# Kernel tuning notes

Measured on AMD Instinct MI355X. Metric: run time of the kernel, lower is better.

## Reference

```python
import jax, jax.numpy as jnp
import numpy as np

NX = 48
N_TILES = 6
C_IN = 16
H = 32            # node_hidden_channels
EH = 64           # edge_hidden_channels
N_STEPS = 4       # num_step_message_passing
N_NODES = N_TILES * NX * NX


def _build_edges(nx, n_tiles):
    # 4-neighbor (up/down/left/right, wraparound) connectivity per tile
    ii = np.arange(nx * nx, dtype=np.int32).reshape(nx, nx)
    srcs, dsts = [], []
    for t in range(n_tiles):
        off = t * nx * nx
        for ax, sh in ((0, 1), (0, -1), (1, 1), (1, -1)):
            srcs.append(off + np.roll(ii, sh, axis=ax).ravel())
            dsts.append(off + ii.ravel())
    return np.concatenate(srcs), np.concatenate(dsts)


def setup_inputs() -> dict:
    key = jax.random.key(0)
    ks = jax.random.split(key, 16)
    src_np, dst_np = _build_edges(NX, N_TILES)
    E = src_np.shape[0]  # 55296
    s = 0.1
    return {
        "in_node_feats": jax.random.normal(ks[0], (2, N_TILES, NX, NX, C_IN), jnp.float32),
        "edge_feats": jax.random.normal(ks[1], (E, 2), jnp.float32),
        "src": jnp.asarray(src_np, jnp.int32),
        "dst": jnp.asarray(dst_np, jnp.int32),
        # project_node_feats: Linear(C_IN,H) -> relu -> Linear(H,H)
        "pW1": jax.random.normal(ks[2], (C_IN, H), jnp.float32) * s,
        "pb1": jnp.zeros((H,), jnp.float32),
        "pW2": jax.random.normal(ks[3], (H, H), jnp.float32) * s,
        "pb2": jnp.zeros((H,), jnp.float32),
        # edge network: Linear(2,EH) -> relu -> Linear(EH, H*H)
        "eW1": jax.random.normal(ks[4], (2, EH), jnp.float32) * s,
        "eb1": jnp.zeros((EH,), jnp.float32),
        "eW2": jax.random.normal(ks[5], (EH, H * H), jnp.float32) * (s / 4.0),
        "eb2": jnp.zeros((H * H,), jnp.float32),
        # NNConv bias
        "conv_b": jnp.zeros((H,), jnp.float32),
        # GRU (single layer): gate order r, z, n (PyTorch)
        "gWih": jax.random.normal(ks[6], (3 * H, H), jnp.float32) * s,
        "gWhh": jax.random.normal(ks[7], (3 * H, H), jnp.float32) * s,
        "gbih": jnp.zeros((3 * H,), jnp.float32),
        "gbhh": jnp.zeros((3 * H,), jnp.float32),
    }


def reference(in_node_feats, edge_feats, src, dst,
              pW1, pb1, pW2, pb2, eW1, eb1, eW2, eb2,
              conv_b, gWih, gWhh, gbih, gbhh):
    shp = in_node_feats.shape           # (B, T, nx, ny, Cin)
    B = shp[0]
    N = shp[1] * shp[2] * shp[3]
    x = in_node_feats.reshape(B, N, shp[-1])
    # project node features
    x = jnp.maximum(x @ pW1 + pb1, 0.0) @ pW2 + pb2      # (B, N, H)
    # per-edge weight matrices (shared across batch and steps)
    We = jnp.maximum(edge_feats @ eW1 + eb1, 0.0) @ eW2 + eb2
    We = We.reshape(-1, H, H)                             # (E, H, H)
    h = x
    seg = jax.vmap(lambda m: jax.ops.segment_sum(m, dst, num_segments=N))
    for _ in range(N_STEPS):
        # NNConv: gather src feats, per-edge matmul, scatter-sum to dst, + bias
        msg = jnp.einsum('beh,eho->beo', x[:, src], We)   # (B, E, H)
        x = jnp.maximum(seg(msg) + conv_b, 0.0)           # relu(conv)
        # GRU cell (seq_len = 1)
        gx = x @ gWih.T + gbih
        gh = h @ gWhh.T + gbhh
        xr, xz, xn = jnp.split(gx, 3, axis=-1)
        hr, hz, hn = jnp.split(gh, 3, axis=-1)
        r = jax.nn.sigmoid(xr + hr)
        z = jax.nn.sigmoid(xz + hz)
        n = jnp.tanh(xn + r * hn)
        h = (1.0 - z) * n + z * h
        x = h
    return x.reshape(shp[:4] + (H,))
```

## Files before the change

### kernel.cpp

```cpp
#include <hip/hip_runtime.h>
#include <stdint.h>

constexpr int NB   = 2;
constexpr int NN   = 13824;
constexpr int NE   = 55296;
constexpr int H    = 32;
constexpr int EHID = 64;
constexpr int HH   = 1024;
constexpr int TILE = 2304;
constexpr int NXC  = 48;

typedef float f32x4 __attribute__((ext_vector_type(4)));
typedef short s16x8 __attribute__((ext_vector_type(8)));
typedef unsigned int u32x2 __attribute__((ext_vector_type(2)));
typedef __attribute__((address_space(1))) unsigned int as1_uint;
typedef __attribute__((address_space(3))) unsigned int as3_uint;

static __device__ __forceinline__ unsigned short f2bf(float f) {
    unsigned u = __float_as_uint(f);
    return (unsigned short)((u + 0x7fffu + ((u >> 16) & 1u)) >> 16);
}
static __device__ __forceinline__ void gload16(const void* g, void* l) {
    __builtin_amdgcn_global_load_lds((const as1_uint*)g, (as3_uint*)l, 16, 0, 0);
}
static __device__ __forceinline__ float sigf(float v) {
    return 1.0f / (1.0f + __expf(-v));
}
static __device__ __forceinline__ float tanhfast(float v) {
    return 1.0f - 2.0f / (1.0f + __expf(2.0f * v));
}

__global__ void __launch_bounds__(256)
k_prep(const float* __restrict__ ef, const float* __restrict__ eW1,
       const float* __restrict__ eb1, unsigned short* __restrict__ aB,
       const float* __restrict__ eW2, const float* __restrict__ eb2,
       unsigned short* __restrict__ BpT, float* __restrict__ eb2p) {
    int blk = blockIdx.x;
    if (blk < 13824) {
        int t = blk * 256 + threadIdx.x;
        int e = t >> 6, k = t & 63;
        float v = ef[e * 2] * eW1[k] + ef[e * 2 + 1] * eW1[64 + k] + eb1[k];
        aB[t] = f2bf(fmaxf(v, 0.f));
    } else {
        int idx = (blk - 13824) * 256 + threadIdx.x;
        int jp = idx & (HH - 1);
        int k  = idx >> 10;
        int src_col = (jp & 31) * 32 + (jp >> 5);
        BpT[jp * EHID + k] = f2bf(eW2[k * HH + src_col]);
        if (k == 0) eb2p[jp] = eb2[src_col];
    }
}

__global__ void __launch_bounds__(256)
k_gemm(const unsigned short* __restrict__ A, const unsigned short* __restrict__ Bt,
       const float* __restrict__ eb2p, unsigned short* __restrict__ C) {
    __shared__ unsigned char lds[32768] __attribute__((aligned(16)));
    const int tid  = threadIdx.x;
    const int wv   = tid >> 6;
    const int lane = tid & 63;
    const int lr   = lane & 15;
    const int lg   = lane >> 4;
    const int nb   = blockIdx.x;
    const int mb   = blockIdx.y;

    const unsigned char* Ag = (const unsigned char*)A  + (size_t)mb * 16384;
    const unsigned char* Bg = (const unsigned char*)Bt + (size_t)nb * 16384;

#pragma unroll
    for (int c = 0; c < 4; c++) {
        int fbase = (wv * 4 + c) * 1024;
        int f  = fbase + lane * 16;
        int sw = f ^ (((f >> 7) & 7) << 4);
        gload16(Ag + sw, lds + fbase);
        gload16(Bg + sw, lds + 16384 + fbase);
    }
    asm volatile("s_waitcnt vmcnt(0)" ::: "memory");
    __syncthreads();

    const int wm = wv >> 1, wn = wv & 1;
    f32x4 acc[4][4] = {};
#pragma unroll
    for (int kk = 0; kk < 2; kk++) {
        s16x8 af[4], bf[4];
#pragma unroll
        for (int i = 0; i < 4; i++) {
            int la = ((wm * 64 + i * 16 + lr) * 64 + kk * 32 + lg * 8) * 2;
            la ^= ((la >> 7) & 7) << 4;
            af[i] = *(const s16x8*)(lds + la);
            int lb = ((wn * 64 + i * 16 + lr) * 64 + kk * 32 + lg * 8) * 2;
            lb ^= ((lb >> 7) & 7) << 4;
            bf[i] = *(const s16x8*)(lds + 16384 + lb);
        }
#pragma unroll
        for (int i = 0; i < 4; i++)
#pragma unroll
            for (int j = 0; j < 4; j++)
                acc[i][j] = __builtin_amdgcn_mfma_f32_16x16x32_bf16(af[i], bf[j], acc[i][j], 0, 0, 0);
    }

#pragma unroll
    for (int j = 0; j < 4; j++) {
        int col = nb * 128 + wn * 64 + j * 16 + lr;
        float bias = eb2p[col];
#pragma unroll
        for (int i = 0; i < 4; i++) {
            int row0 = mb * 128 + wm * 64 + i * 16 + lg * 4;
#pragma unroll
            for (int r = 0; r < 4; r++)
                C[(size_t)(row0 + r) * HH + col] = f2bf(acc[i][j][r] + bias);
        }
    }
}

__global__ void __launch_bounds__(256)
k_proj(const float* __restrict__ in, const float* __restrict__ pW1,
       const float* __restrict__ pb1, const float* __restrict__ pW2,
       const float* __restrict__ pb2, float* __restrict__ S0,
       unsigned short* __restrict__ xb0,
       const float* __restrict__ gWih, const float* __restrict__ gWhh,
       unsigned short* __restrict__ gWb) {
    int blk = blockIdx.x;
    if (blk >= 3456) {
        int idx = (blk - 3456) * 256 + threadIdx.x;
        gWb[idx] = f2bf(idx < 3072 ? gWih[idx] : gWhh[idx - 3072]);
        return;
    }
    int t = blk * 256 + threadIdx.x;
    int p = t >> 5;
    int l = t & 31;
    float iv = (l < 16) ? in[p * 16 + l] : 0.f;
    float hid = pb1[l];
#pragma unroll
    for (int c = 0; c < 16; c++) hid = fmaf(__shfl(iv, c, 32), pW1[c * H + l], hid);
    hid = fmaxf(hid, 0.f);
    float out = pb2[l];
#pragma unroll
    for (int h = 0; h < 32; h++) out = fmaf(__shfl(hid, h, 32), pW2[h * H + l], out);
    S0[p * H + l]  = out;
    xb0[p * H + l] = f2bf(out);
}

__global__ void __launch_bounds__(256)
k_conv(const unsigned short* __restrict__ xb,
       const unsigned short* __restrict__ WeT,
       const float* __restrict__ conv_b,
       unsigned short* __restrict__ cval) {
    const int tid  = threadIdx.x;
    const int wv   = tid >> 6;
    const int l    = tid & 63;
    const int cl   = l & 15;
    const int kg   = l >> 4;
    const int bsel = cl & 1;
    const int n0   = (blockIdx.x * 4 + wv) * 8;

    f32x4 cb0 = *(const f32x4*)(conv_b + kg * 4);
    f32x4 cb1 = *(const f32x4*)(conv_b + 16 + kg * 4);

    for (int u = 0; u < 8; ++u) {
        int n = n0 + u;
        int t = n / TILE;
        int i = n - t * TILE;
        int r = i / NXC;
        int c = i - r * NXC;
        int bt = t * TILE;
        int rm = (r == 0) ? NXC - 1 : r - 1;
        int rp = (r == NXC - 1) ? 0 : r + 1;
        int cm = (c == 0) ? NXC - 1 : c - 1;
        int cp = (c == NXC - 1) ? 0 : c + 1;
        int s0 = bt + rm * NXC + c;
        int s1 = bt + rp * NXC + c;
        int s2 = bt + r * NXC + cm;
        int s3 = bt + r * NXC + cp;
        int ss[4] = {s0, s1, s2, s3};

        f32x4 a0 = {}, a1 = {};
#pragma unroll
        for (int k = 0; k < 4; ++k) {
            size_t e = (size_t)((t * 4 + k) * TILE + i);
            const unsigned short* wp = WeT + e * HH;
            s16x8 af0 = *(const s16x8*)(wp + cl * 32 + kg * 8);
            s16x8 af1 = *(const s16x8*)(wp + 512 + cl * 32 + kg * 8);
            s16x8 bfr = *(const s16x8*)(xb + ((size_t)(bsel * NN + ss[k])) * 32 + kg * 8);
            a0 = __builtin_amdgcn_mfma_f32_16x16x32_bf16(af0, bfr, a0, 0, 0, 0);
            a1 = __builtin_amdgcn_mfma_f32_16x16x32_bf16(af1, bfr, a1, 0, 0, 0);
        }
        if (cl < 2) {
            unsigned short* op = cval + ((size_t)(bsel * NN + n)) * 32 + kg * 4;
            u32x2 p0, p1;
            p0[0] = (unsigned)f2bf(fmaxf(a0[0] + cb0[0], 0.f)) |
                    ((unsigned)f2bf(fmaxf(a0[1] + cb0[1], 0.f)) << 16);
            p0[1] = (unsigned)f2bf(fmaxf(a0[2] + cb0[2], 0.f)) |
                    ((unsigned)f2bf(fmaxf(a0[3] + cb0[3], 0.f)) << 16);
            p1[0] = (unsigned)f2bf(fmaxf(a1[0] + cb1[0], 0.f)) |
                    ((unsigned)f2bf(fmaxf(a1[1] + cb1[1], 0.f)) << 16);
            p1[1] = (unsigned)f2bf(fmaxf(a1[2] + cb1[2], 0.f)) |
                    ((unsigned)f2bf(fmaxf(a1[3] + cb1[3], 0.f)) << 16);
            *(u32x2*)op        = p0;
            *(u32x2*)(op + 16) = p1;
        }
    }
}

__global__ void __launch_bounds__(256)
k_gru(const unsigned short* __restrict__ cval,
      const unsigned short* __restrict__ xbin,
      const float* __restrict__ hin,
      const unsigned short* __restrict__ gWb,
      const float* __restrict__ gbih, const float* __restrict__ gbhh,
      float* __restrict__ hout, unsigned short* __restrict__ xbout) {
    const int tid = threadIdx.x;
    const int wv  = tid >> 6;
    const int l   = tid & 63;
    const int cl  = l & 15;
    const int kg  = l >> 4;
    const int mt  = blockIdx.x * 4 + wv;

    s16x8 ax = *(const s16x8*)(cval + (size_t)mt * 512 + cl * 32 + kg * 8);
    s16x8 ah = *(const s16x8*)(xbin + (size_t)mt * 512 + cl * 32 + kg * 8);

    f32x4 accx[6], acch[6];
#pragma unroll
    for (int jb = 0; jb < 6; ++jb) {
        s16x8 wx = *(const s16x8*)(gWb + (jb * 16 + cl) * 32 + kg * 8);
        s16x8 wh = *(const s16x8*)(gWb + 3072 + (jb * 16 + cl) * 32 + kg * 8);
        f32x4 z0 = {};
        f32x4 z1 = {};
        accx[jb] = __builtin_amdgcn_mfma_f32_16x16x32_bf16(ax, wx, z0, 0, 0, 0);
        acch[jb] = __builtin_amdgcn_mfma_f32_16x16x32_bf16(ah, wh, z1, 0, 0, 0);
    }

    float bihR[2] = {gbih[cl],      gbih[16 + cl]};
    float bihZ[2] = {gbih[32 + cl], gbih[48 + cl]};
    float bihN[2] = {gbih[64 + cl], gbih[80 + cl]};
    float bhhR[2] = {gbhh[cl],      gbhh[16 + cl]};
    float bhhZ[2] = {gbhh[32 + cl], gbhh[48 + cl]};
    float bhhN[2] = {gbhh[64 + cl], gbhh[80 + cl]};

#pragma unroll
    for (int hb = 0; hb < 2; ++hb) {
        const float* hp = hin  + (size_t)mt * 512 + kg * 128 + hb * 16 + cl;
        float*       op = hout + (size_t)mt * 512 + kg * 128 + hb * 16 + cl;
        unsigned short* xp = xbout + (size_t)mt * 512 + kg * 128 + hb * 16 + cl;
#pragma unroll
        for (int ri = 0; ri < 4; ++ri) {
            float rg = sigf(accx[hb][ri] + acch[hb][ri] + bihR[hb] + bhhR[hb]);
            float zg = sigf(accx[2 + hb][ri] + acch[2 + hb][ri] + bihZ[hb] + bhhZ[hb]);
            float ng = tanhfast((accx[4 + hb][ri] + bihN[hb]) +
                                rg * (acch[4 + hb][ri] + bhhN[hb]));
            float ho = hp[ri * 32];
            float hn = fmaf(zg, ho - ng, ng);
            op[ri * 32] = hn;
            xp[ri * 32] = f2bf(hn);
        }
    }
}

extern "C" void kernel_launch(void* const* d_in, const int* in_sizes, int n_in,
                              void* d_out, int out_size, void* d_ws, size_t ws_size,
                              hipStream_t stream) {
    const float* in_nodes = (const float*)d_in[0];
    const float* ef       = (const float*)d_in[1];
    const float* pW1      = (const float*)d_in[4];
    const float* pb1      = (const float*)d_in[5];
    const float* pW2      = (const float*)d_in[6];
    const float* pb2      = (const float*)d_in[7];
    const float* eW1      = (const float*)d_in[8];
    const float* eb1      = (const float*)d_in[9];
    const float* eW2      = (const float*)d_in[10];
    const float* eb2      = (const float*)d_in[11];
    const float* convb    = (const float*)d_in[12];
    const float* gWih     = (const float*)d_in[13];
    const float* gWhh     = (const float*)d_in[14];
    const float* gbih     = (const float*)d_in[15];
    const float* gbhh     = (const float*)d_in[16];

    unsigned char* ws = (unsigned char*)d_ws;
    unsigned short* WeT  = (unsigned short*)(ws + 0ull);
    unsigned short* aB   = (unsigned short*)(ws + 113246208ull);
    unsigned short* xb0  = (unsigned short*)(ws + 113246208ull);
    unsigned short* xb1  = (unsigned short*)(ws + 115015680ull);
    unsigned short* cval = (unsigned short*)(ws + 116785152ull);
    unsigned short* gWb  = (unsigned short*)(ws + 118554624ull);
    unsigned short* BpT  = (unsigned short*)(ws + 120324096ull);
    float*          eb2p = (float*)         (ws + 120455168ull);
    float*          S0   = (float*)         (ws + 120459264ull);
    float*          S1   = (float*)         (ws + 123998208ull);

    k_prep<<<13824 + 256, 256, 0, stream>>>(ef, eW1, eb1, aB, eW2, eb2, BpT, eb2p);
    dim3 g3(8, 432);
    k_gemm<<<g3, 256, 0, stream>>>(aB, BpT, eb2p, WeT);
    k_proj<<<3456 + 24, 256, 0, stream>>>(in_nodes, pW1, pb1, pW2, pb2, S0, xb0,
                                          gWih, gWhh, gWb);

    float* out = (float*)d_out;
    k_conv<<<432, 256, 0, stream>>>(xb0, WeT, convb, cval);
    k_gru <<<432, 256, 0, stream>>>(cval, xb0, S0, gWb, gbih, gbhh, S1, xb1);
    k_conv<<<432, 256, 0, stream>>>(xb1, WeT, convb, cval);
    k_gru <<<432, 256, 0, stream>>>(cval, xb1, S1, gWb, gbih, gbhh, S0, xb0);
    k_conv<<<432, 256, 0, stream>>>(xb0, WeT, convb, cval);
    k_gru <<<432, 256, 0, stream>>>(cval, xb0, S0, gWb, gbih, gbhh, S1, xb1);
    k_conv<<<432, 256, 0, stream>>>(xb1, WeT, convb, cval);
    k_gru <<<432, 256, 0, stream>>>(cval, xb1, S1, gWb, gbih, gbhh, out, xb0);
}
```

Baseline: 246.6 us.

## Fuse NNConv and GRU per step, vectorize prep, stage GEMM output through LDS

```diff
diff --git a/kernel.cpp b/kernel.cpp
--- a/kernel.cpp
+++ b/kernel.cpp
@@ -13,12 +13,16 @@
 typedef float f32x4 __attribute__((ext_vector_type(4)));
 typedef short s16x8 __attribute__((ext_vector_type(8)));
 typedef unsigned int u32x2 __attribute__((ext_vector_type(2)));
+typedef unsigned int u32x4 __attribute__((ext_vector_type(4)));
 typedef __attribute__((address_space(1))) unsigned int as1_uint;
 typedef __attribute__((address_space(3))) unsigned int as3_uint;
 
 static __device__ __forceinline__ unsigned short f2bf(float f) {
     unsigned u = __float_as_uint(f);
     return (unsigned short)((u + 0x7fffu + ((u >> 16) & 1u)) >> 16);
+}
+static __device__ __forceinline__ unsigned packbf(float lo, float hi) {
+    return (unsigned)f2bf(lo) | ((unsigned)f2bf(hi) << 16);
 }
 static __device__ __forceinline__ void gload16(const void* g, void* l) {
     __builtin_amdgcn_global_load_lds((const as1_uint*)g, (as3_uint*)l, 16, 0, 0);
@@ -36,23 +40,36 @@
        const float* __restrict__ eW2, const float* __restrict__ eb2,
        unsigned short* __restrict__ BpT, float* __restrict__ eb2p) {
     int blk = blockIdx.x;
-    if (blk < 13824) {
+    if (blk < 3456) {
         int t = blk * 256 + threadIdx.x;
-        int e = t >> 6, k = t & 63;
-        float v = ef[e * 2] * eW1[k] + ef[e * 2 + 1] * eW1[64 + k] + eb1[k];
-        aB[t] = f2bf(fmaxf(v, 0.f));
+        int e = t >> 4, kq = (t & 15) * 4;
+        float f0 = ef[e * 2], f1 = ef[e * 2 + 1];
+        u32x2 w;
+#pragma unroll
+        for (int q = 0; q < 2; q++) {
+            int k = kq + q * 2;
+            float v0 = fmaxf(f0 * eW1[k]     + f1 * eW1[64 + k]     + eb1[k],     0.f);
+            float v1 = fmaxf(f0 * eW1[k + 1] + f1 * eW1[64 + k + 1] + eb1[k + 1], 0.f);
+            w[q] = packbf(v0, v1);
+        }
+        *(u32x2*)(aB + e * 64 + kq) = w;
     } else {
-        int idx = (blk - 13824) * 256 + threadIdx.x;
-        int jp = idx & (HH - 1);
-        int k  = idx >> 10;
+        int t = (blk - 3456) * 256 + threadIdx.x;
+        int jp = t >> 4, kq = (t & 15) * 4;
         int src_col = (jp & 31) * 32 + (jp >> 5);
-        BpT[jp * EHID + k] = f2bf(eW2[k * HH + src_col]);
-        if (k == 0) eb2p[jp] = eb2[src_col];
+        u32x2 w;
+#pragma unroll
+        for (int q = 0; q < 2; q++) {
+            int k = kq + q * 2;
+            w[q] = packbf(eW2[k * HH + src_col], eW2[(k + 1) * HH + src_col]);
+        }
+        *(u32x2*)(BpT + jp * 64 + kq) = w;
+        if (kq == 0) eb2p[jp] = eb2[src_col];
     }
 }
 
 __global__ void __launch_bounds__(256)
-k_gemm(const unsigned short* __restrict__ A, const unsigned short* __restrict__ Bt,
+k_gemm(const unsigned short* __restrict__ Bp, const unsigned short* __restrict__ Ae,
        const float* __restrict__ eb2p, unsigned short* __restrict__ C) {
     __shared__ unsigned char lds[32768] __attribute__((aligned(16)));
     const int tid  = threadIdx.x;
@@ -60,11 +77,11 @@
     const int lane = tid & 63;
     const int lr   = lane & 15;
     const int lg   = lane >> 4;
-    const int nb   = blockIdx.x;
-    const int mb   = blockIdx.y;
-
-    const unsigned char* Ag = (const unsigned char*)A  + (size_t)mb * 16384;
-    const unsigned char* Bg = (const unsigned char*)Bt + (size_t)nb * 16384;
+    const int jbt  = blockIdx.x;
+    const int ebt  = blockIdx.y;
+
+    const unsigned char* Ag = (const unsigned char*)Bp + (size_t)jbt * 16384;
+    const unsigned char* Bg = (const unsigned char*)Ae + (size_t)ebt * 16384;
 
 #pragma unroll
     for (int c = 0; c < 4; c++) {
@@ -98,17 +115,38 @@
                 acc[i][j] = __builtin_amdgcn_mfma_f32_16x16x32_bf16(af[i], bf[j], acc[i][j], 0, 0, 0);
     }
 
-#pragma unroll
-    for (int j = 0; j < 4; j++) {
-        int col = nb * 128 + wn * 64 + j * 16 + lr;
-        float bias = eb2p[col];
-#pragma unroll
-        for (int i = 0; i < 4; i++) {
-            int row0 = mb * 128 + wm * 64 + i * 16 + lg * 4;
-#pragma unroll
-            for (int r = 0; r < 4; r++)
-                C[(size_t)(row0 + r) * HH + col] = f2bf(acc[i][j][r] + bias);
-        }
+    float bias[4][4];
+#pragma unroll
+    for (int i = 0; i < 4; i++)
+#pragma unroll
+        for (int r = 0; r < 4; r++)
+            bias[i][r] = eb2p[jbt * 128 + wm * 64 + i * 16 + lg * 4 + r];
+
+    __syncthreads();
+#pragma unroll
+    for (int i = 0; i < 4; i++) {
+#pragma unroll
+        for (int j = 0; j < 4; j++) {
+            int el    = wn * 64 + j * 16 + lr;
+            int jbase = wm * 64 + i * 16 + lg * 4;
+            int L0 = el * 256 + jbase * 2;
+            int ph = L0 ^ ((el & 7) << 4);
+            u32x2 w;
+            w[0] = packbf(acc[i][j][0] + bias[i][0], acc[i][j][1] + bias[i][1]);
+            w[1] = packbf(acc[i][j][2] + bias[i][2], acc[i][j][3] + bias[i][3]);
+            *(u32x2*)(lds + ph) = w;
+        }
+    }
+    __syncthreads();
+
+    const size_t cbase = (size_t)(ebt * 128) * 2048 + (size_t)jbt * 256;
+#pragma unroll
+    for (int pass = 0; pass < 8; pass++) {
+        int L2 = pass * 4096 + tid * 16;
+        int el = L2 >> 8;
+        int ph = L2 ^ ((el & 7) << 4);
+        u32x4 v = *(const u32x4*)(lds + ph);
+        *(u32x4*)((unsigned char*)C + cbase + (size_t)el * 2048 + (L2 & 255)) = v;
     }
 }
 
@@ -141,23 +179,27 @@
 }
 
 __global__ void __launch_bounds__(256)
-k_conv(const unsigned short* __restrict__ xb,
-       const unsigned short* __restrict__ WeT,
-       const float* __restrict__ conv_b,
-       unsigned short* __restrict__ cval) {
+k_step2(const unsigned short* __restrict__ xb_in,
+        const float* __restrict__ h_in,
+        const unsigned short* __restrict__ WeT,
+        const float* __restrict__ conv_b,
+        const unsigned short* __restrict__ gWb,
+        const float* __restrict__ gbih, const float* __restrict__ gbhh,
+        float* __restrict__ h_out, unsigned short* __restrict__ xb_out) {
+    __shared__ unsigned short cv[2][16][32];
     const int tid  = threadIdx.x;
     const int wv   = tid >> 6;
     const int l    = tid & 63;
     const int cl   = l & 15;
     const int kg   = l >> 4;
     const int bsel = cl & 1;
-    const int n0   = (blockIdx.x * 4 + wv) * 8;
+    const int n0   = blockIdx.x * 16;
 
     f32x4 cb0 = *(const f32x4*)(conv_b + kg * 4);
     f32x4 cb1 = *(const f32x4*)(conv_b + 16 + kg * 4);
 
-    for (int u = 0; u < 8; ++u) {
-        int n = n0 + u;
+    for (int u = 0; u < 4; ++u) {
+        int n = n0 + wv * 4 + u;
         int t = n / TILE;
         int i = n - t * TILE;
         int r = i / NXC;
@@ -167,11 +209,8 @@
         int rp = (r == NXC - 1) ? 0 : r + 1;
         int cm = (c == 0) ? NXC - 1 : c - 1;
         int cp = (c == NXC - 1) ? 0 : c + 1;
-        int s0 = bt + rm * NXC + c;
-        int s1 = bt + rp * NXC + c;
-        int s2 = bt + r * NXC + cm;
-        int s3 = bt + r * NXC + cp;
-        int ss[4] = {s0, s1, s2, s3};
+        int ss[4] = {bt + rm * NXC + c, bt + rp * NXC + c,
+                     bt + r * NXC + cm, bt + r * NXC + cp};
 
         f32x4 a0 = {}, a1 = {};
 #pragma unroll
@@ -180,77 +219,62 @@
             const unsigned short* wp = WeT + e * HH;
             s16x8 af0 = *(const s16x8*)(wp + cl * 32 + kg * 8);
             s16x8 af1 = *(const s16x8*)(wp + 512 + cl * 32 + kg * 8);
-            s16x8 bfr = *(const s16x8*)(xb + ((size_t)(bsel * NN + ss[k])) * 32 + kg * 8);
+            s16x8 bfr = *(const s16x8*)(xb_in + ((size_t)(bsel * NN + ss[k])) * 32 + kg * 8);
             a0 = __builtin_amdgcn_mfma_f32_16x16x32_bf16(af0, bfr, a0, 0, 0, 0);
             a1 = __builtin_amdgcn_mfma_f32_16x16x32_bf16(af1, bfr, a1, 0, 0, 0);
         }
         if (cl < 2) {
-            unsigned short* op = cval + ((size_t)(bsel * NN + n)) * 32 + kg * 4;
-            u32x2 p0, p1;
-            p0[0] = (unsigned)f2bf(fmaxf(a0[0] + cb0[0], 0.f)) |
-                    ((unsigned)f2bf(fmaxf(a0[1] + cb0[1], 0.f)) << 16);
-            p0[1] = (unsigned)f2bf(fmaxf(a0[2] + cb0[2], 0.f)) |
-                    ((unsigned)f2bf(fmaxf(a0[3] + cb0[3], 0.f)) << 16);
-            p1[0] = (unsigned)f2bf(fmaxf(a1[0] + cb1[0], 0.f)) |
-                    ((unsigned)f2bf(fmaxf(a1[1] + cb1[1], 0.f)) << 16);
-            p1[1] = (unsigned)f2bf(fmaxf(a1[2] + cb1[2], 0.f)) |
-                    ((unsigned)f2bf(fmaxf(a1[3] + cb1[3], 0.f)) << 16);
-            *(u32x2*)op        = p0;
-            *(u32x2*)(op + 16) = p1;
-        }
-    }
-}
-
-__global__ void __launch_bounds__(256)
-k_gru(const unsigned short* __restrict__ cval,
-      const unsigned short* __restrict__ xbin,
-      const float* __restrict__ hin,
-      const unsigned short* __restrict__ gWb,
-      const float* __restrict__ gbih, const float* __restrict__ gbhh,
-      float* __restrict__ hout, unsigned short* __restrict__ xbout) {
-    const int tid = threadIdx.x;
-    const int wv  = tid >> 6;
-    const int l   = tid & 63;
-    const int cl  = l & 15;
-    const int kg  = l >> 4;
-    const int mt  = blockIdx.x * 4 + wv;
-
-    s16x8 ax = *(const s16x8*)(cval + (size_t)mt * 512 + cl * 32 + kg * 8);
-    s16x8 ah = *(const s16x8*)(xbin + (size_t)mt * 512 + cl * 32 + kg * 8);
-
-    f32x4 accx[6], acch[6];
-#pragma unroll
-    for (int jb = 0; jb < 6; ++jb) {
-        s16x8 wx = *(const s16x8*)(gWb + (jb * 16 + cl) * 32 + kg * 8);
-        s16x8 wh = *(const s16x8*)(gWb + 3072 + (jb * 16 + cl) * 32 + kg * 8);
-        f32x4 z0 = {};
-        f32x4 z1 = {};
-        accx[jb] = __builtin_amdgcn_mfma_f32_16x16x32_bf16(ax, wx, z0, 0, 0, 0);
-        acch[jb] = __builtin_amdgcn_mfma_f32_16x16x32_bf16(ah, wh, z1, 0, 0, 0);
-    }
-
-    float bihR[2] = {gbih[cl],      gbih[16 + cl]};
-    float bihZ[2] = {gbih[32 + cl], gbih[48 + cl]};
-    float bihN[2] = {gbih[64 + cl], gbih[80 + cl]};
-    float bhhR[2] = {gbhh[cl],      gbhh[16 + cl]};
-    float bhhZ[2] = {gbhh[32 + cl], gbhh[48 + cl]};
-    float bhhN[2] = {gbhh[64 + cl], gbhh[80 + cl]};
-
-#pragma unroll
-    for (int hb = 0; hb < 2; ++hb) {
-        const float* hp = hin  + (size_t)mt * 512 + kg * 128 + hb * 16 + cl;
-        float*       op = hout + (size_t)mt * 512 + kg * 128 + hb * 16 + cl;
-        unsigned short* xp = xbout + (size_t)mt * 512 + kg * 128 + hb * 16 + cl;
-#pragma unroll
-        for (int ri = 0; ri < 4; ++ri) {
-            float rg = sigf(accx[hb][ri] + acch[hb][ri] + bihR[hb] + bhhR[hb]);
-            float zg = sigf(accx[2 + hb][ri] + acch[2 + hb][ri] + bihZ[hb] + bhhZ[hb]);
-            float ng = tanhfast((accx[4 + hb][ri] + bihN[hb]) +
-                                rg * (acch[4 + hb][ri] + bhhN[hb]));
-            float ho = hp[ri * 32];
-            float hn = fmaf(zg, ho - ng, ng);
-            op[ri * 32] = hn;
-            xp[ri * 32] = f2bf(hn);
+            int nl = wv * 4 + u;
+            unsigned* cp32 = (unsigned*)&cv[cl][nl][0];
+            cp32[kg * 2]     = packbf(fmaxf(a0[0] + cb0[0], 0.f), fmaxf(a0[1] + cb0[1], 0.f));
+            cp32[kg * 2 + 1] = packbf(fmaxf(a0[2] + cb0[2], 0.f), fmaxf(a0[3] + cb0[3], 0.f));
+            cp32[8 + kg * 2]     = packbf(fmaxf(a1[0] + cb1[0], 0.f), fmaxf(a1[1] + cb1[1], 0.f));
+            cp32[8 + kg * 2 + 1] = packbf(fmaxf(a1[2] + cb1[2], 0.f), fmaxf(a1[3] + cb1[3], 0.f));
+        }
+    }
+    __syncthreads();
+
+    if (wv < 2) {
+        const int b = wv;
+        const size_t mbase = (size_t)b * NN + n0;
+
+        s16x8 ax = *(const s16x8*)&cv[b][cl][kg * 8];
+        s16x8 ah = *(const s16x8*)(xb_in + (mbase + cl) * 32 + kg * 8);
+
+        f32x4 accx[6], acch[6];
+#pragma unroll
+        for (int jb = 0; jb < 6; ++jb) {
+            s16x8 wx = *(const s16x8*)(gWb + (jb * 16 + cl) * 32 + kg * 8);
+            s16x8 wh = *(const s16x8*)(gWb + 3072 + (jb * 16 + cl) * 32 + kg * 8);
+            f32x4 z0 = {};
+            f32x4 z1 = {};
+            accx[jb] = __builtin_amdgcn_mfma_f32_16x16x32_bf16(ax, wx, z0, 0, 0, 0);
+            acch[jb] = __builtin_amdgcn_mfma_f32_16x16x32_bf16(ah, wh, z1, 0, 0, 0);
+        }
+
+        float bihR[2] = {gbih[cl],      gbih[16 + cl]};
+        float bihZ[2] = {gbih[32 + cl], gbih[48 + cl]};
+        float bihN[2] = {gbih[64 + cl], gbih[80 + cl]};
+        float bhhR[2] = {gbhh[cl],      gbhh[16 + cl]};
+        float bhhZ[2] = {gbhh[32 + cl], gbhh[48 + cl]};
+        float bhhN[2] = {gbhh[64 + cl], gbhh[80 + cl]};
+
+#pragma unroll
+        for (int hb = 0; hb < 2; ++hb) {
+            const float* hp = h_in  + mbase * 32 + kg * 128 + hb * 16 + cl;
+            float*       op = h_out + mbase * 32 + kg * 128 + hb * 16 + cl;
+            unsigned short* xp = xb_out + mbase * 32 + kg * 128 + hb * 16 + cl;
+#pragma unroll
+            for (int ri = 0; ri < 4; ++ri) {
+                float rg = sigf(accx[hb][ri] + acch[hb][ri] + bihR[hb] + bhhR[hb]);
+                float zg = sigf(accx[2 + hb][ri] + acch[2 + hb][ri] + bihZ[hb] + bhhZ[hb]);
+                float ng = tanhfast((accx[4 + hb][ri] + bihN[hb]) +
+                                    rg * (acch[4 + hb][ri] + bhhN[hb]));
+                float ho = hp[ri * 32];
+                float hn = fmaf(zg, ho - ng, ng);
+                op[ri * 32] = hn;
+                xp[ri * 32] = f2bf(hn);
+            }
         }
     }
 }
@@ -279,26 +303,21 @@
     unsigned short* aB   = (unsigned short*)(ws + 113246208ull);
     unsigned short* xb0  = (unsigned short*)(ws + 113246208ull);
     unsigned short* xb1  = (unsigned short*)(ws + 115015680ull);
-    unsigned short* cval = (unsigned short*)(ws + 116785152ull);
     unsigned short* gWb  = (unsigned short*)(ws + 118554624ull);
     unsigned short* BpT  = (unsigned short*)(ws + 120324096ull);
     float*          eb2p = (float*)         (ws + 120455168ull);
     float*          S0   = (float*)         (ws + 120459264ull);
     float*          S1   = (float*)         (ws + 123998208ull);
 
-    k_prep<<<13824 + 256, 256, 0, stream>>>(ef, eW1, eb1, aB, eW2, eb2, BpT, eb2p);
+    k_prep<<<3456 + 64, 256, 0, stream>>>(ef, eW1, eb1, aB, eW2, eb2, BpT, eb2p);
     dim3 g3(8, 432);
-    k_gemm<<<g3, 256, 0, stream>>>(aB, BpT, eb2p, WeT);
+    k_gemm<<<g3, 256, 0, stream>>>(BpT, aB, eb2p, WeT);
     k_proj<<<3456 + 24, 256, 0, stream>>>(in_nodes, pW1, pb1, pW2, pb2, S0, xb0,
                                           gWih, gWhh, gWb);
 
     float* out = (float*)d_out;
-    k_conv<<<432, 256, 0, stream>>>(xb0, WeT, convb, cval);
-    k_gru <<<432, 256, 0, stream>>>(cval, xb0, S0, gWb, gbih, gbhh, S1, xb1);
-    k_conv<<<432, 256, 0, stream>>>(xb1, WeT, convb, cval);
-    k_gru <<<432, 256, 0, stream>>>(cval, xb1, S1, gWb, gbih, gbhh, S0, xb0);
-    k_conv<<<432, 256, 0, stream>>>(xb0, WeT, convb, cval);
-    k_gru <<<432, 256, 0, stream>>>(cval, xb0, S0, gWb, gbih, gbhh, S1, xb1);
-    k_conv<<<432, 256, 0, stream>>>(xb1, WeT, convb, cval);
-    k_gru <<<432, 256, 0, stream>>>(cval, xb1, S1, gWb, gbih, gbhh, out, xb0);
-}
+    k_step2<<<864, 256, 0, stream>>>(xb0, S0, WeT, convb, gWb, gbih, gbhh, S1, xb1);
+    k_step2<<<864, 256, 0, stream>>>(xb1, S1, WeT, convb, gWb, gbih, gbhh, S0, xb0);
+    k_step2<<<864, 256, 0, stream>>>(xb0, S0, WeT, convb, gWb, gbih, gbhh, S1, xb1);
+    k_step2<<<864, 256, 0, stream>>>(xb1, S1, WeT, convb, gWb, gbih, gbhh, out, xb0);
+}
```

Measured after the change: 219.3 us. 1.12x faster.
